# Performance work log

Hardware: AMD Instinct MI355X
Metric: run time of the kernel (lower is better)

Reference implementation:

```python
import jax, jax.numpy as jnp
import numpy as np

GAMMA = 9.6
BETA = 0.83
LAMDA = 10.0
EPS = 1e-12

B, D, C = 1024, 512, 10000


def _l2norm(x):
    # torch F.normalize: x / max(||x||_2, eps)
    n = jnp.sqrt(jnp.sum(x * x, axis=1, keepdims=True))
    return x / jnp.maximum(n, EPS)


def setup_inputs() -> dict:
    key = jax.random.key(0)
    k1, k2, k3, k4 = jax.random.split(key, 4)
    inp = jax.random.normal(k1, (B, D), dtype=jnp.float32)
    # xavier-uniform-like init for the classifier weight
    limit = float(np.sqrt(6.0 / (C + D)))
    weight = jax.random.uniform(k2, (C, D), dtype=jnp.float32, minval=-limit, maxval=limit)
    class_weight = jax.random.uniform(k3, (C,), dtype=jnp.float32)  # per-class margins in [0,1)
    label = jax.random.randint(k4, (B,), 0, C, dtype=jnp.int32)
    return {"input": inp, "weight": weight, "class_weight": class_weight, "label": label}


def reference(input, weight, class_weight, label):
    x = _l2norm(input)            # [B, D]
    w = _l2norm(weight)           # [C, D]
    fea = x @ w.T                 # [B, C] cosine logits

    # sp_i = fea[i, label_i]; logit_{ij} = sn_ij - sp_i + beta * m_j  (j != label_i)
    sp = jnp.take_along_axis(fea, label[:, None], axis=1)           # [B, 1]
    logits = GAMMA * (fea - sp + BETA * class_weight[None, :])      # [B, C]
    pos_mask = label[:, None] == jnp.arange(C, dtype=label.dtype)[None, :]
    logits = jnp.where(pos_mask, -jnp.inf, logits)                  # drop positive column
    lse = jax.scipy.special.logsumexp(logits, axis=1)               # [B]
    loss = jax.nn.softplus(lse)                                     # [B]

    # inter-class similarity penalty
    score = jnp.clip(w @ w.T, -1.0, 1.0)                            # [C, C]
    score = score * (1.0 - jnp.eye(C, dtype=score.dtype))           # zero diagonal
    s = jnp.max(score[label], axis=1)                               # [B]
    loss_w = jax.nn.softplus(jnp.mean(s) + 0.5)

    loss = loss + LAMDA * loss_w
    return fea, jnp.mean(loss)
```

## Files before the change

kernel.cpp:

```cpp
#include <hip/hip_runtime.h>
#include <math.h>

#define GAMMA 9.6f
#define BETA  0.83f
#define LAMDA 10.0f
#define B_ 1024
#define D_ 512
#define C_ 10000
#define M0_ 20.0f

#define WS_XB   0
#define WS_WB   1048576
#define WS_SU   11288576
#define WS_T    11292672
#define WS_SP   11296768

typedef __attribute__((ext_vector_type(8))) short short8;
typedef __attribute__((ext_vector_type(4))) float floatx4;

__device__ __forceinline__ unsigned enc_f(float f) {
    unsigned i = __float_as_uint(f);
    return (i & 0x80000000u) ? ~i : (i | 0x80000000u);
}
__device__ __forceinline__ float dec_f(unsigned u) {
    return (u & 0x80000000u) ? __uint_as_float(u ^ 0x80000000u)
                             : __uint_as_float(~u);
}
__device__ __forceinline__ float softplus_f(float x) {
    return (x > 30.f) ? x : log1pf(expf(x));
}
__device__ __forceinline__ unsigned short f2bf_rne(float f) {
    unsigned u = __float_as_uint(f);
    u += 0x7FFFu + ((u >> 16) & 1u);
    return (unsigned short)(u >> 16);
}

__global__ __launch_bounds__(128) void normcvt_kernel(
    const float* __restrict__ input, const float* __restrict__ weight,
    unsigned short* __restrict__ xb, unsigned short* __restrict__ wb,
    unsigned* __restrict__ s_u, float* __restrict__ T) {
    int row = blockIdx.x;
    int tid = threadIdx.x;
    if (row < B_ && tid == 0) { s_u[row] = 0u; T[row] = 0.f; }

    const float* src = (row < B_) ? (input + (size_t)row * D_)
                                  : (weight + (size_t)(row - B_) * D_);
    float4 v = *(const float4*)(src + tid * 4);
    float ss = v.x * v.x + v.y * v.y + v.z * v.z + v.w * v.w;
    #pragma unroll
    for (int o = 32; o > 0; o >>= 1) ss += __shfl_xor(ss, o, 64);
    __shared__ float red[2];
    if ((tid & 63) == 0) red[tid >> 6] = ss;
    __syncthreads();
    float inv = 1.0f / fmaxf(sqrtf(red[0] + red[1]), 1e-12f);
    unsigned short* dst = (row < B_) ? (xb + (size_t)row * D_)
                                     : (wb + (size_t)(row - B_) * D_);
    ushort4 o4;
    o4.x = f2bf_rne(v.x * inv);
    o4.y = f2bf_rne(v.y * inv);
    o4.z = f2bf_rne(v.z * inv);
    o4.w = f2bf_rne(v.w * inv);
    *(ushort4*)(dst + tid * 4) = o4;
}

#define BM 128
#define BN 256
#define BK 32
#define NSTEP (D_ / BK)
#define NTILE_M 16
#define NTILE_N 40
#define NWG (NTILE_M * NTILE_N)

__global__ __launch_bounds__(512, 4) void mfma_gemm_kernel(
    const unsigned short* __restrict__ xb, const unsigned short* __restrict__ wb,
    const int* __restrict__ label, const float* __restrict__ cw,
    float* __restrict__ fea, unsigned* __restrict__ s_u,
    float* __restrict__ T, float* __restrict__ sp) {
    __shared__ __align__(16) unsigned short As[2][BM * BK];
    __shared__ __align__(16) unsigned short Bs[2][BN * BK];

    const int tid = threadIdx.x;
    const int orig = (blockIdx.x & 7) * (NWG / 8) + (blockIdx.x >> 3);
    const int m0 = (orig & 15) * BM;
    const int n0 = (orig >> 4) * BN;
    const bool feaTile = (m0 < B_);

    const int srow = tid >> 2;
    const int kc8 = (tid & 3) * 8;
    const unsigned short* asrc;
    {
        int rm = m0 + srow;
        if (rm < B_) asrc = xb + (size_t)rm * D_ + kc8;
        else         asrc = wb + (size_t)label[rm - B_] * D_ + kc8;
    }
    const unsigned short* bsrc[2];
    #pragma unroll
    for (int q = 0; q < 2; q++) {
        int rn = n0 + srow + q * 128;
        if (rn >= C_) rn = C_ - 1;
        bsrc[q] = wb + (size_t)rn * D_ + kc8;
    }

    const int lane = tid & 63;
    const int wv = tid >> 6;
    const int wvr = (wv >> 2) * 64;
    const int wvc = (wv & 3) * 64;
    const int l15 = lane & 15;
    const int hi = lane >> 4;

    floatx4 acc[4][4];
    #pragma unroll
    for (int i = 0; i < 4; i++)
        #pragma unroll
        for (int j = 0; j < 4; j++)
            acc[i][j] = (floatx4){0.f, 0.f, 0.f, 0.f};

#define STAGE(buf, kt)                                                         \
    {                                                                          \
        __builtin_amdgcn_global_load_lds(                                      \
            (const __attribute__((address_space(1))) void*)(asrc + (kt)),      \
            (__attribute__((address_space(3))) void*)((char*)&As[buf][0] + tid * 16), \
            16, 0, 0);                                                         \
        _Pragma("unroll")                                                      \
        for (int q = 0; q < 2; q++) {                                          \
            __builtin_amdgcn_global_load_lds(                                  \
                (const __attribute__((address_space(1))) void*)(bsrc[q] + (kt)),\
                (__attribute__((address_space(3))) void*)((char*)&Bs[buf][0] + tid * 16 + q * 8192), \
                16, 0, 0);                                                     \
        }                                                                      \
    }

    STAGE(0, 0);
    __syncthreads();

    int cur = 0;
    for (int t = 0; t < NSTEP; ++t) {
        int ktn = (t + 1) * BK;
        if (ktn < D_) STAGE(cur ^ 1, ktn);
        short8 a[4], b[4];
        #pragma unroll
        for (int i = 0; i < 4; i++)
            a[i] = *(const short8*)&As[cur][(wvr + i * 16 + l15) * BK + hi * 8];
        #pragma unroll
        for (int j = 0; j < 4; j++)
            b[j] = *(const short8*)&Bs[cur][(wvc + j * 16 + l15) * BK + hi * 8];
        #pragma unroll
        for (int i = 0; i < 4; i++)
            #pragma unroll
            for (int j = 0; j < 4; j++)
                acc[i][j] = __builtin_amdgcn_mfma_f32_16x16x32_bf16(
                    a[i], b[j], acc[i][j], 0, 0, 0);
        __syncthreads();
        cur ^= 1;
    }

    if (feaTile) {
        int lbl_ir[4][4];
        #pragma unroll
        for (int i = 0; i < 4; i++)
            #pragma unroll
            for (int r = 0; r < 4; r++)
                lbl_ir[i][r] = label[m0 + wvr + i * 16 + hi * 4 + r];
        float cwj[4];
        #pragma unroll
        for (int j = 0; j < 4; j++) {
            int n = n0 + wvc + j * 16 + l15;
            cwj[j] = (n < C_) ? cw[n] : 0.f;
        }
        float rs[4][4];
        #pragma unroll
        for (int i = 0; i < 4; i++)
            #pragma unroll
            for (int r = 0; r < 4; r++) rs[i][r] = 0.f;

        #pragma unroll
        for (int i = 0; i < 4; i++) {
            #pragma unroll
            for (int j = 0; j < 4; j++) {
                int n = n0 + wvc + j * 16 + l15;
                if (n < C_) {
                    int m = m0 + wvr + i * 16 + hi * 4;
                    float* dst = fea + (size_t)m * C_ + n;
                    #pragma unroll
                    for (int r = 0; r < 4; r++) {
                        float v = acc[i][j][r];
                        dst[(size_t)r * C_] = v;
                        int l = lbl_ir[i][r];
                        if (n == l) sp[m + r] = v;
                        else rs[i][r] += expf(GAMMA * (v + BETA * cwj[j]) - M0_);
                    }
                }
            }
        }
        #pragma unroll
        for (int i = 0; i < 4; i++) {
            #pragma unroll
            for (int r = 0; r < 4; r++) {
                float s = rs[i][r];
                #pragma unroll
                for (int o = 8; o > 0; o >>= 1) s += __shfl_xor(s, o, 64);
                if (l15 == 0)
                    atomicAdd(T + (m0 + wvr + i * 16 + hi * 4 + r), s);
            }
        }
    } else {
        #pragma unroll
        for (int i = 0; i < 4; i++) {
            #pragma unroll
            for (int r = 0; r < 4; r++) {
                int row = m0 - B_ + wvr + i * 16 + hi * 4 + r;
                int l = label[row];
                float vmax = -2.f;
                #pragma unroll
                for (int j = 0; j < 4; j++) {
                    int n = n0 + wvc + j * 16 + l15;
                    float v = fminf(fmaxf(acc[i][j][r], -1.f), 1.f);
                    if (n == l) v = 0.f;
                    if (n < C_) vmax = fmaxf(vmax, v);
                }
                #pragma unroll
                for (int o = 8; o > 0; o >>= 1)
                    vmax = fmaxf(vmax, __shfl_xor(vmax, o, 64));
                if (l15 == 0) atomicMax(s_u + row, enc_f(vmax));
            }
        }
    }
}

__global__ __launch_bounds__(1024) void final_kernel(
    const unsigned* __restrict__ s_u, const float* __restrict__ T,
    const float* __restrict__ sp, float* __restrict__ out_loss) {
    int tid = threadIdx.x;
    float lse = M0_ + logf(T[tid]) - GAMMA * sp[tid];
    float lr = softplus_f(lse);
    float sv = dec_f(s_u[tid]);
    #pragma unroll
    for (int o = 32; o > 0; o >>= 1) {
        lr += __shfl_xor(lr, o, 64);
        sv += __shfl_xor(sv, o, 64);
    }
    __shared__ float red_l[16], red_s[16];
    if ((tid & 63) == 0) { red_l[tid >> 6] = lr; red_s[tid >> 6] = sv; }
    __syncthreads();
    if (tid == 0) {
        float tl = 0.f, ts = 0.f;
        #pragma unroll
        for (int wv = 0; wv < 16; wv++) { tl += red_l[wv]; ts += red_s[wv]; }
        float loss_w = softplus_f(ts / (float)B_ + 0.5f);
        *out_loss = tl / (float)B_ + LAMDA * loss_w;
    }
}

extern "C" void kernel_launch(void* const* d_in, const int* in_sizes, int n_in,
                              void* d_out, int out_size, void* d_ws, size_t ws_size,
                              hipStream_t stream) {
    const float* input  = (const float*)d_in[0];
    const float* weight = (const float*)d_in[1];
    const float* cw     = (const float*)d_in[2];
    const int*   label  = (const int*)d_in[3];
    float* out = (float*)d_out;

    char* ws = (char*)d_ws;
    unsigned short* xb = (unsigned short*)(ws + WS_XB);
    unsigned short* wb = (unsigned short*)(ws + WS_WB);
    unsigned* s_u      = (unsigned*)(ws + WS_SU);
    float*    T        = (float*)(ws + WS_T);
    float*    sp       = (float*)(ws + WS_SP);

    normcvt_kernel<<<B_ + C_, 128, 0, stream>>>(input, weight, xb, wb, s_u, T);

    mfma_gemm_kernel<<<NWG, 512, 0, stream>>>(xb, wb, label, cw, out, s_u, T, sp);

    final_kernel<<<1, 1024, 0, stream>>>(s_u, T, sp, out + (size_t)B_ * C_);
}
```

Baseline: 71.10 us.

## Halve GEMM N-tile to 128 and fold final reduction into last-finishing block

The GEMM tile drops from 128x256 with 512 threads to 128x128 with 256 threads, which roughly doubles the number of workgroups (1264) to balance load across CUs. The separate final-loss kernel is removed. Instead, each GEMM block bumps a global counter, and the last block to finish computes the loss reduction. This saves one kernel launch but costs an extra atomic and fence per block, and B-tile reuse per block is lower.

```diff
diff --git a/kernel.cpp b/kernel.cpp
--- a/kernel.cpp
+++ b/kernel.cpp
@@ -14,6 +14,7 @@
 #define WS_SU   11288576
 #define WS_T    11292672
 #define WS_SP   11296768
+#define WS_CNT  11300864
 
 typedef __attribute__((ext_vector_type(8))) short short8;
 typedef __attribute__((ext_vector_type(4))) float floatx4;
@@ -38,10 +39,11 @@
 __global__ __launch_bounds__(128) void normcvt_kernel(
     const float* __restrict__ input, const float* __restrict__ weight,
     unsigned short* __restrict__ xb, unsigned short* __restrict__ wb,
-    unsigned* __restrict__ s_u, float* __restrict__ T) {
+    unsigned* __restrict__ s_u, float* __restrict__ T, unsigned* __restrict__ cnt) {
     int row = blockIdx.x;
     int tid = threadIdx.x;
     if (row < B_ && tid == 0) { s_u[row] = 0u; T[row] = 0.f; }
+    if (row == 0 && tid == 1) *cnt = 0u;
 
     const float* src = (row < B_) ? (input + (size_t)row * D_)
                                   : (weight + (size_t)(row - B_) * D_);
@@ -64,20 +66,21 @@
 }
 
 #define BM 128
-#define BN 256
+#define BN 128
 #define BK 32
 #define NSTEP (D_ / BK)
 #define NTILE_M 16
-#define NTILE_N 40
+#define NTILE_N 79
 #define NWG (NTILE_M * NTILE_N)
 
-__global__ __launch_bounds__(512, 4) void mfma_gemm_kernel(
+__global__ __launch_bounds__(256) void mfma_gemm_kernel(
     const unsigned short* __restrict__ xb, const unsigned short* __restrict__ wb,
     const int* __restrict__ label, const float* __restrict__ cw,
     float* __restrict__ fea, unsigned* __restrict__ s_u,
-    float* __restrict__ T, float* __restrict__ sp) {
+    float* __restrict__ T, float* __restrict__ sp,
+    unsigned* __restrict__ cnt, float* __restrict__ out_loss) {
     __shared__ __align__(16) unsigned short As[2][BM * BK];
-    __shared__ __align__(16) unsigned short Bs[2][BN * BK];
+    __shared__ __align__(16) unsigned short Bs[2][BM * BK];
 
     const int tid = threadIdx.x;
     const int orig = (blockIdx.x & 7) * (NWG / 8) + (blockIdx.x >> 3);
@@ -85,26 +88,26 @@
     const int n0 = (orig >> 4) * BN;
     const bool feaTile = (m0 < B_);
 
-    const int srow = tid >> 2;
+    const int arow = tid >> 2;
     const int kc8 = (tid & 3) * 8;
-    const unsigned short* asrc;
-    {
-        int rm = m0 + srow;
-        if (rm < B_) asrc = xb + (size_t)rm * D_ + kc8;
-        else         asrc = wb + (size_t)label[rm - B_] * D_ + kc8;
-    }
+    const unsigned short* asrc[2];
     const unsigned short* bsrc[2];
     #pragma unroll
     for (int q = 0; q < 2; q++) {
-        int rn = n0 + srow + q * 128;
+        int rm = m0 + arow + q * 64;
+        const unsigned short* ab;
+        if (rm < B_) ab = xb + (size_t)rm * D_;
+        else         ab = wb + (size_t)label[rm - B_] * D_;
+        asrc[q] = ab + kc8;
+        int rn = n0 + arow + q * 64;
         if (rn >= C_) rn = C_ - 1;
         bsrc[q] = wb + (size_t)rn * D_ + kc8;
     }
 
     const int lane = tid & 63;
     const int wv = tid >> 6;
-    const int wvr = (wv >> 2) * 64;
-    const int wvc = (wv & 3) * 64;
+    const int wr = (wv >> 1) * 64;
+    const int wc = (wv & 1) * 64;
     const int l15 = lane & 15;
     const int hi = lane >> 4;
 
@@ -117,15 +120,15 @@
 
 #define STAGE(buf, kt)                                                         \
     {                                                                          \
-        __builtin_amdgcn_global_load_lds(                                      \
-            (const __attribute__((address_space(1))) void*)(asrc + (kt)),      \
-            (__attribute__((address_space(3))) void*)((char*)&As[buf][0] + tid * 16), \
-            16, 0, 0);                                                         \
         _Pragma("unroll")                                                      \
         for (int q = 0; q < 2; q++) {                                          \
             __builtin_amdgcn_global_load_lds(                                  \
+                (const __attribute__((address_space(1))) void*)(asrc[q] + (kt)),\
+                (__attribute__((address_space(3))) void*)((char*)&As[buf][0] + tid * 16 + q * 4096), \
+                16, 0, 0);                                                     \
+            __builtin_amdgcn_global_load_lds(                                  \
                 (const __attribute__((address_space(1))) void*)(bsrc[q] + (kt)),\
-                (__attribute__((address_space(3))) void*)((char*)&Bs[buf][0] + tid * 16 + q * 8192), \
+                (__attribute__((address_space(3))) void*)((char*)&Bs[buf][0] + tid * 16 + q * 4096), \
                 16, 0, 0);                                                     \
         }                                                                      \
     }
@@ -140,10 +143,10 @@
         short8 a[4], b[4];
         #pragma unroll
         for (int i = 0; i < 4; i++)
-            a[i] = *(const short8*)&As[cur][(wvr + i * 16 + l15) * BK + hi * 8];
+            a[i] = *(const short8*)&As[cur][(wr + i * 16 + l15) * BK + hi * 8];
         #pragma unroll
         for (int j = 0; j < 4; j++)
-            b[j] = *(const short8*)&Bs[cur][(wvc + j * 16 + l15) * BK + hi * 8];
+            b[j] = *(const short8*)&Bs[cur][(wc + j * 16 + l15) * BK + hi * 8];
         #pragma unroll
         for (int i = 0; i < 4; i++)
             #pragma unroll
@@ -160,11 +163,11 @@
         for (int i = 0; i < 4; i++)
             #pragma unroll
             for (int r = 0; r < 4; r++)
-                lbl_ir[i][r] = label[m0 + wvr + i * 16 + hi * 4 + r];
+                lbl_ir[i][r] = label[m0 + wr + i * 16 + hi * 4 + r];
         float cwj[4];
         #pragma unroll
         for (int j = 0; j < 4; j++) {
-            int n = n0 + wvc + j * 16 + l15;
+            int n = n0 + wc + j * 16 + l15;
             cwj[j] = (n < C_) ? cw[n] : 0.f;
         }
         float rs[4][4];
@@ -177,9 +180,9 @@
         for (int i = 0; i < 4; i++) {
             #pragma unroll
             for (int j = 0; j < 4; j++) {
-                int n = n0 + wvc + j * 16 + l15;
+                int n = n0 + wc + j * 16 + l15;
                 if (n < C_) {
-                    int m = m0 + wvr + i * 16 + hi * 4;
+                    int m = m0 + wr + i * 16 + hi * 4;
                     float* dst = fea + (size_t)m * C_ + n;
                     #pragma unroll
                     for (int r = 0; r < 4; r++) {
@@ -200,7 +203,7 @@
                 #pragma unroll
                 for (int o = 8; o > 0; o >>= 1) s += __shfl_xor(s, o, 64);
                 if (l15 == 0)
-                    atomicAdd(T + (m0 + wvr + i * 16 + hi * 4 + r), s);
+                    atomicAdd(T + (m0 + wr + i * 16 + hi * 4 + r), s);
             }
         }
     } else {
@@ -208,12 +211,12 @@
         for (int i = 0; i < 4; i++) {
             #pragma unroll
             for (int r = 0; r < 4; r++) {
-                int row = m0 - B_ + wvr + i * 16 + hi * 4 + r;
+                int row = m0 - B_ + wr + i * 16 + hi * 4 + r;
                 int l = label[row];
                 float vmax = -2.f;
                 #pragma unroll
                 for (int j = 0; j < 4; j++) {
-                    int n = n0 + wvc + j * 16 + l15;
+                    int n = n0 + wc + j * 16 + l15;
                     float v = fminf(fmaxf(acc[i][j][r], -1.f), 1.f);
                     if (n == l) v = 0.f;
                     if (n < C_) vmax = fmaxf(vmax, v);
@@ -225,29 +228,33 @@
             }
         }
     }
-}
-
-__global__ __launch_bounds__(1024) void final_kernel(
-    const unsigned* __restrict__ s_u, const float* __restrict__ T,
-    const float* __restrict__ sp, float* __restrict__ out_loss) {
-    int tid = threadIdx.x;
-    float lse = M0_ + logf(T[tid]) - GAMMA * sp[tid];
-    float lr = softplus_f(lse);
-    float sv = dec_f(s_u[tid]);
-    #pragma unroll
-    for (int o = 32; o > 0; o >>= 1) {
-        lr += __shfl_xor(lr, o, 64);
-        sv += __shfl_xor(sv, o, 64);
-    }
-    __shared__ float red_l[16], red_s[16];
-    if ((tid & 63) == 0) { red_l[tid >> 6] = lr; red_s[tid >> 6] = sv; }
-    __syncthreads();
-    if (tid == 0) {
-        float tl = 0.f, ts = 0.f;
-        #pragma unroll
-        for (int wv = 0; wv < 16; wv++) { tl += red_l[wv]; ts += red_s[wv]; }
-        float loss_w = softplus_f(ts / (float)B_ + 0.5f);
-        *out_loss = tl / (float)B_ + LAMDA * loss_w;
+
+    __syncthreads();
+    __threadfence();
+    __shared__ unsigned done_s;
+    if (tid == 0) done_s = atomicAdd(cnt, 1u);
+    __syncthreads();
+    if (done_s == NWG - 1) {
+        __threadfence();
+        float lr = 0.f, sv = 0.f;
+        for (int r = tid; r < B_; r += 256) {
+            lr += softplus_f(M0_ + logf(T[r]) - GAMMA * sp[r]);
+            sv += dec_f(s_u[r]);
+        }
+        #pragma unroll
+        for (int o = 32; o > 0; o >>= 1) {
+            lr += __shfl_xor(lr, o, 64);
+            sv += __shfl_xor(sv, o, 64);
+        }
+        __shared__ float red_l[4], red_s[4];
+        if ((tid & 63) == 0) { red_l[tid >> 6] = lr; red_s[tid >> 6] = sv; }
+        __syncthreads();
+        if (tid == 0) {
+            float tl = red_l[0] + red_l[1] + red_l[2] + red_l[3];
+            float ts = red_s[0] + red_s[1] + red_s[2] + red_s[3];
+            float loss_w = softplus_f(ts / (float)B_ + 0.5f);
+            *out_loss = tl / (float)B_ + LAMDA * loss_w;
+        }
     }
 }
 
@@ -266,10 +273,10 @@
     unsigned* s_u      = (unsigned*)(ws + WS_SU);
     float*    T        = (float*)(ws + WS_T);
     float*    sp       = (float*)(ws + WS_SP);
-
-    normcvt_kernel<<<B_ + C_, 128, 0, stream>>>(input, weight, xb, wb, s_u, T);
-
-    mfma_gemm_kernel<<<NWG, 512, 0, stream>>>(xb, wb, label, cw, out, s_u, T, sp);
-
-    final_kernel<<<1, 1024, 0, stream>>>(s_u, T, sp, out + (size_t)B_ * C_);
-}
+    unsigned* cnt      = (unsigned*)(ws + WS_CNT);
+
+    normcvt_kernel<<<B_ + C_, 128, 0, stream>>>(input, weight, xb, wb, s_u, T, cnt);
+
+    mfma_gemm_kernel<<<NWG, 256, 0, stream>>>(xb, wb, label, cw, out, s_u, T, sp,
+                                              cnt, out + (size_t)B_ * C_);
+}
```

Result: slower. 182.0 us (+156.0%).
